# Optimization experiments

Measured on AMD Instinct MI355X. Metric: run time of the kernel, lower is better.

## Reference

```python
import jax, jax.numpy as jnp
import numpy as np

B, N, G, M = 16, 8192, 512, 32
ENC = 384   # encoder_dims
TRD = 384   # trans_dim (must equal ENC due to cls-pos concat)
EPS = 1e-5


def _fps(xyz, n_samples):
    # farthest point sampling: xyz [B,N,3] -> idx [B,n_samples] int32
    b, n, _ = xyz.shape
    def body(carry, _):
        dists, farthest = carry                       # [B,N], [B]
        centroid = jnp.take_along_axis(xyz, farthest[:, None, None], axis=1)  # [B,1,3]
        d = jnp.sum((xyz - centroid) ** 2, -1)        # [B,N]
        dists = jnp.minimum(dists, d)
        nxt = jnp.argmax(dists, -1).astype(jnp.int32)
        return (dists, nxt), farthest
    init = (jnp.full((b, n), 1e10, xyz.dtype), jnp.zeros((b,), jnp.int32))
    _, idxs = jax.lax.scan(body, init, None, length=n_samples)
    return idxs.T                                     # [B,n_samples]


def _group(pts):
    # FPS centers + kNN neighborhoods, neighborhood recentered on its center
    fps_idx = _fps(pts, G)                                    # [B,G]
    center = jax.vmap(lambda p, i: p[i])(pts, fps_idx)        # [B,G,3]
    d2 = jnp.sum((center[:, :, None, :] - pts[:, None, :, :]) ** 2, -1)  # [B,G,N]
    _, knn_idx = jax.lax.top_k(-d2, M)                        # [B,G,M]
    nbhd = jax.vmap(lambda p, i: p[i])(pts, knn_idx)          # [B,G,M,3]
    nbhd = nbhd - center[:, :, None, :]
    return nbhd, center


def _bn(x, g, b, m, v):
    return (x - m) * jax.lax.rsqrt(v + EPS) * g + b


def _forward(pts, W1, b1, g1, be1, m1, v1, W2, b2,
             W3, b3, g2, be2, m2, v2, W4, b4,
             Wp1, bp1, Wp2, bp2, cls_pos):
    nbhd, center = _group(pts)                                # [B,G,M,3], [B,G,3]
    # Encoder (Point-MAE, BN in eval mode)
    f = jnp.einsum('bgmc,cd->bgmd', nbhd, W1) + b1            # [B,G,M,128]
    f = jax.nn.relu(_bn(f, g1, be1, m1, v1))
    f = jnp.einsum('bgmc,cd->bgmd', f, W2) + b2               # [B,G,M,256]
    fg = jnp.max(f, axis=2, keepdims=True)                    # [B,G,1,256]
    f = jnp.concatenate([jnp.broadcast_to(fg, f.shape), f], -1)  # [B,G,M,512]
    f = jnp.einsum('bgmc,cd->bgmd', f, W3) + b3
    f = jax.nn.relu(_bn(f, g2, be2, m2, v2))
    f = jnp.einsum('bgmc,cd->bgmd', f, W4) + b4               # [B,G,M,ENC]
    x = jnp.max(f, axis=2)                                    # [B,G,ENC]
    # pos embed MLP on centers
    pos = jax.nn.gelu(center @ Wp1 + bp1) @ Wp2 + bp2         # [B,G,TRD]
    cls = jnp.broadcast_to(cls_pos, (pts.shape[0], 1, ENC))
    pos = jnp.concatenate([cls, pos], axis=1)                 # [B,G+1,TRD]
    return x, pos


def setup_inputs() -> dict:
    key = jax.random.key(0)
    ks = jax.random.split(key, 20)
    nrm = lambda k, s, sc: jax.random.normal(k, s, jnp.float32) * sc
    uni = lambda k, s: jax.random.uniform(k, s, jnp.float32, 0.5, 1.5)
    return {
        'pts': jax.random.normal(ks[0], (B, N, 3), jnp.float32),
        'W1': nrm(ks[1], (3, 128), 0.1), 'b1': jnp.zeros((128,), jnp.float32),
        'g1': uni(ks[2], (128,)), 'be1': nrm(ks[3], (128,), 0.1),
        'm1': nrm(ks[4], (128,), 0.1), 'v1': uni(ks[5], (128,)),
        'W2': nrm(ks[6], (128, 256), 0.05), 'b2': jnp.zeros((256,), jnp.float32),
        'W3': nrm(ks[7], (512, 512), 0.04), 'b3': jnp.zeros((512,), jnp.float32),
        'g2': uni(ks[8], (512,)), 'be2': nrm(ks[9], (512,), 0.1),
        'm2': nrm(ks[10], (512,), 0.1), 'v2': uni(ks[11], (512,)),
        'W4': nrm(ks[12], (512, ENC), 0.04), 'b4': jnp.zeros((ENC,), jnp.float32),
        'Wp1': nrm(ks[13], (3, 128), 0.1), 'bp1': jnp.zeros((128,), jnp.float32),
        'Wp2': nrm(ks[14], (128, TRD), 0.08), 'bp2': jnp.zeros((TRD,), jnp.float32),
        'cls_pos': nrm(ks[15], (1, 1, ENC), 0.02),
    }


def reference(pts, W1, b1, g1, be1, m1, v1, W2, b2, W3, b3, g2, be2, m2, v2,
              W4, b4, Wp1, bp1, Wp2, bp2, cls_pos):
    return _forward(pts, W1, b1, g1, be1, m1, v1, W2, b2, W3, b3, g2, be2,
                    m2, v2, W4, b4, Wp1, bp1, Wp2, bp2, cls_pos)
```

## Files before the change

### kernel.cpp

```cpp
#include <hip/hip_runtime.h>

typedef _Float16 f16;
typedef _Float16 f16x8 __attribute__((ext_vector_type(8)));
typedef float    f32x4 __attribute__((ext_vector_type(4)));

#define NB   16
#define NP   8192
#define NG   512
#define NM   32
#define ENC  384
#define NROWS (NB * NG * NM)

__device__ __forceinline__ void gl_lds16(const void* g, void* l) {
  __builtin_amdgcn_global_load_lds((const __attribute__((address_space(1))) unsigned int*)g,
                                   (__attribute__((address_space(3))) unsigned int*)l, 16, 0, 0);
}

__device__ __forceinline__ unsigned long long kmax(unsigned long long a, unsigned long long b) {
  return a > b ? a : b;
}
__device__ __forceinline__ unsigned long long kmin(unsigned long long a, unsigned long long b) {
  return a < b ? a : b;
}

template <int CTRL>
__device__ __forceinline__ unsigned long long dpp_kmax(unsigned long long k) {
  int lo = (int)(unsigned)(k & 0xFFFFFFFFull);
  int hi = (int)(unsigned)(k >> 32);
  int olo = __builtin_amdgcn_update_dpp(lo, lo, CTRL, 0xF, 0xF, false);
  int ohi = __builtin_amdgcn_update_dpp(hi, hi, CTRL, 0xF, 0xF, false);
  unsigned long long o = ((unsigned long long)(unsigned)ohi << 32) | (unsigned)olo;
  return kmax(k, o);
}
template <int CTRL>
__device__ __forceinline__ unsigned long long dpp_kmin(unsigned long long k) {
  int lo = (int)(unsigned)(k & 0xFFFFFFFFull);
  int hi = (int)(unsigned)(k >> 32);
  int olo = __builtin_amdgcn_update_dpp(lo, lo, CTRL, 0xF, 0xF, false);
  int ohi = __builtin_amdgcn_update_dpp(hi, hi, CTRL, 0xF, 0xF, false);
  unsigned long long o = ((unsigned long long)(unsigned)ohi << 32) | (unsigned)olo;
  return kmin(k, o);
}
__device__ __forceinline__ unsigned long long swz16_kmax(unsigned long long k) {
  int lo = (int)(unsigned)(k & 0xFFFFFFFFull);
  int hi = (int)(unsigned)(k >> 32);
  int olo = __builtin_amdgcn_ds_swizzle(lo, 0x401F);
  int ohi = __builtin_amdgcn_ds_swizzle(hi, 0x401F);
  unsigned long long o = ((unsigned long long)(unsigned)ohi << 32) | (unsigned)olo;
  return kmax(k, o);
}
__device__ __forceinline__ unsigned long long swz16_kmin(unsigned long long k) {
  int lo = (int)(unsigned)(k & 0xFFFFFFFFull);
  int hi = (int)(unsigned)(k >> 32);
  int olo = __builtin_amdgcn_ds_swizzle(lo, 0x401F);
  int ohi = __builtin_amdgcn_ds_swizzle(hi, 0x401F);
  unsigned long long o = ((unsigned long long)(unsigned)ohi << 32) | (unsigned)olo;
  return kmin(k, o);
}

#define DPP_QUAD_XOR1 0xB1
#define DPP_QUAD_XOR2 0x4E
#define DPP_HALF_MIRR 0x141
#define DPP_ROW_MIRR  0x140

__global__ __launch_bounds__(512) void fps_kernel(const float* __restrict__ pts,
                                                  float* __restrict__ centers) {
#pragma clang fp contract(off)
  const int b = blockIdx.x;
  const float* pb = pts + (size_t)b * NP * 3;
  const int t = threadIdx.x;
  const int lane = t & 63, wid = t >> 6;
  __shared__ float spx[NP], spy[NP], spz[NP];
  __shared__ unsigned long long swk[2][16];
  float px[16], py[16], pz[16], dd[16];
#pragma unroll
  for (int i = 0; i < 16; ++i) {
    int idx = t + i * 512;
    float x = pb[idx * 3 + 0], y = pb[idx * 3 + 1], z = pb[idx * 3 + 2];
    px[i] = x; py[i] = y; pz[i] = z; dd[i] = 1e10f;
    spx[idx] = x; spy[idx] = y; spz[idx] = z;
  }
  __syncthreads();
  float cx = spx[0], cy = spy[0], cz = spz[0];
  for (int g = 0; g < NG; ++g) {
    if (t == 0) {
      float* c = centers + ((size_t)b * NG + g) * 3;
      c[0] = cx; c[1] = cy; c[2] = cz;
    }
    float best = -1.0f; int bslot = 0;
#pragma unroll
    for (int i = 0; i < 16; ++i) {
      float dx = __fsub_rn(px[i], cx);
      float dy = __fsub_rn(py[i], cy);
      float dz = __fsub_rn(pz[i], cz);
      float d  = __fadd_rn(__fadd_rn(__fmul_rn(dx, dx), __fmul_rn(dy, dy)), __fmul_rn(dz, dz));
      dd[i] = fminf(dd[i], d);
      if (dd[i] > best) { best = dd[i]; bslot = i; }
    }
    int bidx = t + bslot * 512;
    unsigned long long key =
        ((unsigned long long)__float_as_uint(best) << 13) | (unsigned)(8191 - bidx);
    key = dpp_kmax<DPP_QUAD_XOR1>(key);
    key = dpp_kmax<DPP_QUAD_XOR2>(key);
    key = dpp_kmax<DPP_HALF_MIRR>(key);
    key = dpp_kmax<DPP_ROW_MIRR>(key);
    key = swz16_kmax(key);
    const int p = g & 1;
    if ((lane & 31) == 0) swk[p][wid * 2 + (lane >> 5)] = key;
    __syncthreads();
    unsigned long long k2 = swk[p][lane & 15];
    k2 = dpp_kmax<DPP_QUAD_XOR1>(k2);
    k2 = dpp_kmax<DPP_QUAD_XOR2>(k2);
    k2 = dpp_kmax<DPP_HALF_MIRR>(k2);
    k2 = dpp_kmax<DPP_ROW_MIRR>(k2);
    int widx = 8191 - (int)(k2 & 0x1FFFull);
    cx = spx[widx]; cy = spy[widx]; cz = spz[widx];
  }
}

__global__ __launch_bounds__(256) void knn_kernel(const float* __restrict__ pts,
                                                  const float* __restrict__ centers,
                                                  int* __restrict__ knn_idx) {
#pragma clang fp contract(off)
  const int gg = blockIdx.x;
  const int b = gg >> 9;
  const float* pb = pts + (size_t)b * NP * 3;
  const float* c = centers + (size_t)gg * 3;
  const float cx = c[0], cy = c[1], cz = c[2];
  __shared__ unsigned long long swk[2][8];
  const int t = threadIdx.x, lane = t & 63, wid = t >> 6;
  float d[32];
  float lmin = 3e38f; int lidx = 0;
#pragma unroll
  for (int i = 0; i < 32; ++i) {
    int idx = i * 256 + t;
    float dx = __fsub_rn(cx, pb[idx * 3 + 0]);
    float dy = __fsub_rn(cy, pb[idx * 3 + 1]);
    float dz = __fsub_rn(cz, pb[idx * 3 + 2]);
    d[i] = __fadd_rn(__fadd_rn(__fmul_rn(dx, dx), __fmul_rn(dy, dy)), __fmul_rn(dz, dz));
    if (d[i] < lmin) { lmin = d[i]; lidx = idx; }
  }
  int* outp = knn_idx + (size_t)gg * NM;
  for (int r = 0; r < NM; ++r) {
    unsigned long long key =
        ((unsigned long long)__float_as_uint(lmin) << 13) | (unsigned)lidx;
    key = dpp_kmin<DPP_QUAD_XOR1>(key);
    key = dpp_kmin<DPP_QUAD_XOR2>(key);
    key = dpp_kmin<DPP_HALF_MIRR>(key);
    key = dpp_kmin<DPP_ROW_MIRR>(key);
    key = swz16_kmin(key);
    const int p = r & 1;
    if ((lane & 31) == 0) swk[p][wid * 2 + (lane >> 5)] = key;
    __syncthreads();
    unsigned long long k2 = swk[p][lane & 7];
    k2 = dpp_kmin<DPP_QUAD_XOR1>(k2);
    k2 = dpp_kmin<DPP_QUAD_XOR2>(k2);
    k2 = dpp_kmin<DPP_HALF_MIRR>(k2);
    int i0 = (int)(k2 & 0x1FFFull);
    if (t == 0) outp[r] = i0;
    if ((i0 & 255) == t) {
      int slot = i0 >> 8;
      lmin = 3e38f; lidx = 0;
#pragma unroll
      for (int i = 0; i < 32; ++i) {
        float di = (i == slot) ? 3e38f : d[i];
        d[i] = di;
        if (di < lmin) { lmin = di; lidx = i * 256 + t; }
      }
    }
  }
}

__global__ void quant_kernel(const float* __restrict__ W2, const float* __restrict__ W3,
                             const float* __restrict__ W4, const float* __restrict__ Wp2,
                             const float* __restrict__ b1, const float* __restrict__ g1,
                             const float* __restrict__ be1, const float* __restrict__ m1,
                             const float* __restrict__ v1, const float* __restrict__ g2,
                             const float* __restrict__ be2, const float* __restrict__ m2,
                             const float* __restrict__ v2,
                             f16* __restrict__ W2T, f16* __restrict__ W3aT,
                             f16* __restrict__ W3bT, f16* __restrict__ W4T,
                             f16* __restrict__ Wp2T,
                             float* __restrict__ s1, float* __restrict__ sh1,
                             float* __restrict__ s2, float* __restrict__ sh2) {
  int i = blockIdx.x * 256 + threadIdx.x;
  if (i < 32768) { int n = i >> 7, k = i & 127; W2T[i] = (f16)W2[(size_t)k * 256 + n]; return; }
  i -= 32768;
  if (i < 131072) { int n = i >> 8, k = i & 255; W3aT[i] = (f16)W3[(size_t)k * 512 + n]; return; }
  i -= 131072;
  if (i < 131072) { int n = i >> 8, k = i & 255; W3bT[i] = (f16)W3[(size_t)(256 + k) * 512 + n]; return; }
  i -= 131072;
  if (i < 196608) { int n = i >> 9, k = i & 511; W4T[i] = (f16)W4[(size_t)k * 384 + n]; return; }
  i -= 196608;
  if (i < 49152) { int n = i >> 7, k = i & 127; Wp2T[i] = (f16)Wp2[(size_t)k * 384 + n]; return; }
  i -= 49152;
  if (i < 128) {
    float s = g1[i] * rsqrtf(v1[i] + 1e-5f);
    s1[i] = s; sh1[i] = (b1[i] - m1[i]) * s + be1[i];
    return;
  }
  i -= 128;
  if (i < 512) {
    float s = g2[i] * rsqrtf(v2[i] + 1e-5f);
    s2[i] = s; sh2[i] = be2[i] - m2[i] * s;
    return;
  }
}

template <int WRITE_F2>
__global__ __launch_bounds__(256) void l2f_kernel(const float* __restrict__ pts,
                                                  const float* __restrict__ centers,
                                                  const int* __restrict__ knn_idx,
                                                  const float* __restrict__ W1,
                                                  const float* __restrict__ s1,
                                                  const float* __restrict__ sh1,
                                                  const f16* __restrict__ W2T,
                                                  const float* __restrict__ b2,
                                                  f16* __restrict__ fg,
                                                  f16* __restrict__ f2, int grow0) {
  __shared__ __align__(16) f16 sF1[128 * 128];
  __shared__ float snb[128][3];
  const int t = threadIdx.x, lane = t & 63, wid = t >> 6;
  const int wr = wid >> 1, wc = wid & 1;
  const int l15 = lane & 15, lhi = lane >> 4;
  const int grow = grow0 + blockIdx.x * 128;
  const int y = blockIdx.y;

  if (t < 128) {
    int row = grow + t;
    int gg = row >> 5;
    int b = gg >> 9;
    int idx = knn_idx[(size_t)gg * NM + (row & 31)];
    const float* p = pts + ((size_t)b * NP + idx) * 3;
    const float* c = centers + (size_t)gg * 3;
    snb[t][0] = p[0] - c[0];
    snb[t][1] = p[1] - c[1];
    snb[t][2] = p[2] - c[2];
  }
  __syncthreads();
  {
    int row = t >> 1, c0 = (t & 1) * 64;
    float nx = snb[row][0], ny = snb[row][1], nz = snb[row][2];
    int sw = (row & 7) << 4;
#pragma unroll
    for (int cc = 0; cc < 64; cc += 8) {
      f16x8 v;
#pragma unroll
      for (int j = 0; j < 8; ++j) {
        int c = c0 + cc + j;
        float a = nx * W1[c] + ny * W1[128 + c] + nz * W1[256 + c];
        a = a * s1[c] + sh1[c];
        v[j] = (f16)fmaxf(a, 0.0f);
      }
      *(f16x8*)((char*)sF1 + row * 256 + (((c0 + cc) * 2) ^ sw)) = v;
    }
  }
  __syncthreads();

  f32x4 acc[4][4];
#pragma unroll
  for (int m = 0; m < 4; ++m)
#pragma unroll
    for (int n = 0; n < 4; ++n) acc[m][n] = (f32x4){0.f, 0.f, 0.f, 0.f};

  const f16* Wb = W2T + (size_t)(y * 128) * 128;
#pragma unroll
  for (int ks = 0; ks < 4; ++ks) {
    f16x8 af[4], bf[4];
#pragma unroll
    for (int m = 0; m < 4; ++m) {
      int row = wr * 64 + m * 16 + l15;
      af[m] = *(const f16x8*)((const char*)sF1 + row * 256 + ((ks * 64 + lhi * 16) ^ ((row & 7) << 4)));
    }
#pragma unroll
    for (int n = 0; n < 4; ++n) {
      int nr = wc * 64 + n * 16 + l15;
      bf[n] = *(const f16x8*)(Wb + (size_t)nr * 128 + ks * 32 + lhi * 8);
    }
#pragma unroll
    for (int m = 0; m < 4; ++m)
#pragma unroll
      for (int n = 0; n < 4; ++n)
        acc[m][n] = __builtin_amdgcn_mfma_f32_16x16x32_f16(af[m], bf[n], acc[m][n], 0, 0, 0);
  }

  float bias[4];
#pragma unroll
  for (int n = 0; n < 4; ++n) bias[n] = b2[y * 128 + wc * 64 + n * 16 + l15];
#pragma unroll
  for (int p = 0; p < 2; ++p) {
#pragma unroll
    for (int n = 0; n < 4; ++n) {
      float v = acc[2 * p][n][0];
#pragma unroll
      for (int i = 1; i < 4; ++i) v = fmaxf(v, acc[2 * p][n][i]);
#pragma unroll
      for (int i = 0; i < 4; ++i) v = fmaxf(v, acc[2 * p + 1][n][i]);
      v = fmaxf(v, __shfl_xor(v, 16));
      v = fmaxf(v, __shfl_xor(v, 32));
      if (lhi == 0)
        fg[(size_t)((grow >> 5) + wr * 2 + p) * 256 + y * 128 + wc * 64 + n * 16 + l15] =
            (f16)(v + bias[n]);
    }
  }

  if (WRITE_F2) {
    __syncthreads();
    f16* sF2 = sF1;
#pragma unroll
    for (int n = 0; n < 4; ++n) {
      int col = wc * 64 + n * 16 + l15;
#pragma unroll
      for (int m = 0; m < 4; ++m)
#pragma unroll
        for (int i = 0; i < 4; ++i) {
          int row = wr * 64 + m * 16 + lhi * 4 + i;
          sF2[row * 128 + col] = (f16)(acc[m][n][i] + bias[n]);
        }
    }
    __syncthreads();
#pragma unroll
    for (int ch = 0; ch < 8; ++ch) {
      int off = ch * 4096 + t * 16;
      int row = off >> 8, cb = off & 255;
      *(uint4*)((char*)f2 + (size_t)(blockIdx.x * 128 + row) * 512 + y * 256 + cb) =
          *(const uint4*)((const char*)sF2 + off);
    }
  }
}

template <int K, int EPI>
__global__ __launch_bounds__(256) void gemm128_kernel(const f16* __restrict__ A,
                                                      const f16* __restrict__ BT,
                                                      float* __restrict__ outF32,
                                                      f16* __restrict__ outF16,
                                                      const float* __restrict__ e0,
                                                      const float* __restrict__ e1,
                                                      const float* __restrict__ e2,
                                                      int NTOT, int gg0) {
  __shared__ __align__(16) f16 sA[128 * 64];
  __shared__ __align__(16) f16 sB[128 * 64];
  const int t = threadIdx.x, lane = t & 63, wid = t >> 6;
  const int wrow = wid >> 1, wcol = wid & 1;
  const int l15 = lane & 15, lhi = lane >> 4;
  f32x4 acc[4][4];
#pragma unroll
  for (int m = 0; m < 4; ++m)
#pragma unroll
    for (int n = 0; n < 4; ++n) acc[m][n] = (f32x4){0.f, 0.f, 0.f, 0.f};

  const size_t arow0 = (size_t)blockIdx.x * 128;
  const int ncol0 = blockIdx.y * 128;
  const char* Ab = (const char*)A;
  const char* Bb = (const char*)BT;
  const int so = wid * 1024 + lane * 16;
  const int cb = so & 127;
  const int r0 = so >> 7;

  for (int kt = 0; kt < K; kt += 64) {
#pragma unroll
    for (int rnd = 0; rnd < 4; ++rnd) {
      int r = rnd * 32 + r0;
      int sw = (r & 7) << 4;
      gl_lds16(Ab + (arow0 + r) * (size_t)(K * 2) + kt * 2 + (cb ^ sw),
               (char*)sA + rnd * 4096 + wid * 1024);
      gl_lds16(Bb + (size_t)(ncol0 + r) * (K * 2) + kt * 2 + (cb ^ sw),
               (char*)sB + rnd * 4096 + wid * 1024);
    }
    __syncthreads();
#pragma unroll
    for (int ks = 0; ks < 2; ++ks) {
      f16x8 af[4], bf[4];
#pragma unroll
      for (int m = 0; m < 4; ++m) {
        int row = wrow * 64 + m * 16 + l15;
        int addr = row * 128 + ((ks * 64 + lhi * 16) ^ ((row & 7) << 4));
        af[m] = *(const f16x8*)((const char*)sA + addr);
      }
#pragma unroll
      for (int n = 0; n < 4; ++n) {
        int nrow = wcol * 64 + n * 16 + l15;
        int addr = nrow * 128 + ((ks * 64 + lhi * 16) ^ ((nrow & 7) << 4));
        bf[n] = *(const f16x8*)((const char*)sB + addr);
      }
#pragma unroll
      for (int m = 0; m < 4; ++m)
#pragma unroll
        for (int n = 0; n < 4; ++n)
          acc[m][n] = __builtin_amdgcn_mfma_f32_16x16x32_f16(af[m], bf[n], acc[m][n], 0, 0, 0);
    }
    __syncthreads();
  }

  if (EPI == 1) {
#pragma unroll
    for (int n = 0; n < 4; ++n) {
      int col = ncol0 + wcol * 64 + n * 16 + l15;
      float s = e1[col], sh = e2[col];
#pragma unroll
      for (int m = 0; m < 4; ++m) {
        int grp = gg0 + blockIdx.x * 4 + wrow * 2 + (m >> 1);
        float gv = e0[(size_t)grp * 512 + col];
#pragma unroll
        for (int i = 0; i < 4; ++i) {
          size_t row = arow0 + wrow * 64 + m * 16 + lhi * 4 + i;
          float v = (acc[m][n][i] + gv) * s + sh;
          outF16[row * NTOT + col] = (f16)fmaxf(v, 0.0f);
        }
      }
    }
  } else if (EPI == 2) {
#pragma unroll
    for (int pr = 0; pr < 2; ++pr) {
      size_t gg_glob = (size_t)gg0 + blockIdx.x * 4 + wrow * 2 + pr;
#pragma unroll
      for (int n = 0; n < 4; ++n) {
        float v = acc[2 * pr][n][0];
#pragma unroll
        for (int i = 1; i < 4; ++i) v = fmaxf(v, acc[2 * pr][n][i]);
#pragma unroll
        for (int i = 0; i < 4; ++i) v = fmaxf(v, acc[2 * pr + 1][n][i]);
        v = fmaxf(v, __shfl_xor(v, 16));
        v = fmaxf(v, __shfl_xor(v, 32));
        if (lhi == 0) {
          int col = ncol0 + wcol * 64 + n * 16 + l15;
          outF32[gg_glob * ENC + col] = v + e0[col];
        }
      }
    }
  } else if (EPI == 3) {
#pragma unroll
    for (int n = 0; n < 4; ++n) {
      int col = ncol0 + wcol * 64 + n * 16 + l15;
      float bias = e0[col];
#pragma unroll
      for (int m = 0; m < 4; ++m)
#pragma unroll
        for (int i = 0; i < 4; ++i) {
          size_t row = arow0 + wrow * 64 + m * 16 + lhi * 4 + i;
          outF32[row * NTOT + col] = acc[m][n][i] + bias;
        }
    }
  } else {
#pragma unroll
    for (int n = 0; n < 4; ++n) {
      int col = ncol0 + wcol * 64 + n * 16 + l15;
      float bias = e0[col];
#pragma unroll
      for (int m = 0; m < 4; ++m)
#pragma unroll
        for (int i = 0; i < 4; ++i) {
          size_t row = arow0 + wrow * 64 + m * 16 + lhi * 4 + i;
          int b = (int)(row >> 9), g = (int)(row & 511);
          outF32[((size_t)b * 513 + 1 + g) * 384 + col] = acc[m][n][i] + bias;
        }
    }
  }
}

__global__ __launch_bounds__(256) void posh_kernel(const float* __restrict__ centers,
                                                   const float* __restrict__ Wp1,
                                                   const float* __restrict__ bp1,
                                                   f16* __restrict__ h) {
  int o = blockIdx.x * 256 + threadIdx.x;
  int row = o >> 7, c = o & 127;
  const float* ct = centers + (size_t)row * 3;
  float x = ct[0] * Wp1[c] + ct[1] * Wp1[128 + c] + ct[2] * Wp1[256 + c] + bp1[c];
  float u = 0.7978845608028654f * (x + 0.044715f * x * x * x);
  h[o] = (f16)(0.5f * x * (1.0f + tanhf(u)));
}

__global__ void cls_kernel(const float* __restrict__ cls_pos, float* __restrict__ out_pos) {
  out_pos[(size_t)blockIdx.x * (NG + 1) * ENC + threadIdx.x] = cls_pos[threadIdx.x];
}

extern "C" void kernel_launch(void* const* d_in, const int* in_sizes, int n_in,
                              void* d_out, int out_size, void* d_ws, size_t ws_size,
                              hipStream_t stream) {
  const float* pts = (const float*)d_in[0];
  const float* W1  = (const float*)d_in[1];
  const float* b1  = (const float*)d_in[2];
  const float* g1  = (const float*)d_in[3];
  const float* be1 = (const float*)d_in[4];
  const float* m1  = (const float*)d_in[5];
  const float* v1  = (const float*)d_in[6];
  const float* W2  = (const float*)d_in[7];
  const float* b2  = (const float*)d_in[8];
  const float* W3  = (const float*)d_in[9];
  const float* b3  = (const float*)d_in[10];
  const float* g2  = (const float*)d_in[11];
  const float* be2 = (const float*)d_in[12];
  const float* m2  = (const float*)d_in[13];
  const float* v2  = (const float*)d_in[14];
  const float* W4  = (const float*)d_in[15];
  const float* b4  = (const float*)d_in[16];
  const float* Wp1 = (const float*)d_in[17];
  const float* bp1 = (const float*)d_in[18];
  const float* Wp2 = (const float*)d_in[19];
  const float* bp2 = (const float*)d_in[20];
  const float* cls = (const float*)d_in[21];

  float* out_x   = (float*)d_out;
  float* out_pos = out_x + (size_t)NB * NG * ENC;

  char* w = (char*)d_ws;
  auto alloc = [&](size_t bytes) {
    char* p = w;
    w += (bytes + 255) & ~(size_t)255;
    return p;
  };
  float* centers = (float*)alloc((size_t)NB * NG * 3 * 4);
  int*   knn     = (int*)alloc((size_t)NB * NG * NM * 4);
  f16*   W2T     = (f16*)alloc(32768 * 2);
  f16*   W3aT    = (f16*)alloc(131072 * 2);
  f16*   W3bT    = (f16*)alloc(131072 * 2);
  f16*   W4T     = (f16*)alloc(196608 * 2);
  f16*   Wp2T    = (f16*)alloc(49152 * 2);
  float* s1      = (float*)alloc(128 * 4);
  float* sh1     = (float*)alloc(128 * 4);
  float* s2      = (float*)alloc(512 * 4);
  float* sh2     = (float*)alloc(512 * 4);
  f16*   fg      = (f16*)alloc((size_t)8192 * 256 * 2);
  float* g3      = (float*)alloc((size_t)8192 * 512 * 4);
  f16*   h       = (f16*)alloc((size_t)8192 * 128 * 2);
  size_t fixed = (size_t)(w - (char*)d_ws);
  const size_t f2_full = (size_t)NROWS * 256 * 2;
  const size_t f3_full = (size_t)NROWS * 512 * 2;

  quant_kernel<<<dim3(2115), dim3(256), 0, stream>>>(W2, W3, W4, Wp2, b1, g1, be1, m1, v1,
                                                     g2, be2, m2, v2, W2T, W3aT, W3bT, W4T,
                                                     Wp2T, s1, sh1, s2, sh2);
  fps_kernel<<<dim3(NB), dim3(512), 0, stream>>>(pts, centers);
  knn_kernel<<<dim3(NB * NG), dim3(256), 0, stream>>>(pts, centers, knn);

  if (ws_size >= fixed + f2_full + f3_full / 4 + 4096) {
    f16* f2  = (f16*)alloc(f2_full);
    f16* f3c = (f16*)alloc(f3_full / 4);
    l2f_kernel<1><<<dim3(2048, 2), dim3(256), 0, stream>>>(pts, centers, knn, W1, s1, sh1,
                                                           W2T, b2, fg, f2, 0);
    gemm128_kernel<256, 3><<<dim3(64, 4), dim3(256), 0, stream>>>(
        fg, W3aT, g3, nullptr, b3, nullptr, nullptr, 512, 0);
    for (int c = 0; c < 4; ++c) {
      gemm128_kernel<256, 1><<<dim3(512, 4), dim3(256), 0, stream>>>(
          f2 + (size_t)c * 65536 * 256, W3bT, nullptr, f3c, g3, s2, sh2, 512, c * 2048);
      gemm128_kernel<512, 2><<<dim3(512, 3), dim3(256), 0, stream>>>(
          f3c, W4T, out_x, nullptr, b4, nullptr, nullptr, 384, c * 2048);
    }
  } else {
    f16* f2c = (f16*)alloc((size_t)32768 * 256 * 2);
    f16* f3c = (f16*)alloc((size_t)32768 * 512 * 2);
    l2f_kernel<0><<<dim3(2048, 2), dim3(256), 0, stream>>>(pts, centers, knn, W1, s1, sh1,
                                                           W2T, b2, fg, nullptr, 0);
    gemm128_kernel<256, 3><<<dim3(64, 4), dim3(256), 0, stream>>>(
        fg, W3aT, g3, nullptr, b3, nullptr, nullptr, 512, 0);
    for (int c = 0; c < 8; ++c) {
      l2f_kernel<1><<<dim3(256, 2), dim3(256), 0, stream>>>(pts, centers, knn, W1, s1, sh1,
                                                            W2T, b2, fg, f2c, c * 32768);
      gemm128_kernel<256, 1><<<dim3(256, 4), dim3(256), 0, stream>>>(
          f2c, W3bT, nullptr, f3c, g3, s2, sh2, 512, c * 1024);
      gemm128_kernel<512, 2><<<dim3(256, 3), dim3(256), 0, stream>>>(
          f3c, W4T, out_x, nullptr, b4, nullptr, nullptr, 384, c * 1024);
    }
  }

  posh_kernel<<<dim3(4096), dim3(256), 0, stream>>>(centers, Wp1, bp1, h);
  gemm128_kernel<128, 4><<<dim3(64, 3), dim3(256), 0, stream>>>(
      h, Wp2T, out_pos, nullptr, bp2, nullptr, nullptr, 384, 0);
  cls_kernel<<<dim3(NB), dim3(ENC), 0, stream>>>(cls, out_pos);
}
```

Before: 1.185 ms.

## Double-buffer GEMM LDS tiles and process encoder rows in larger chunks

The 128x128 MFMA GEMM now keeps two LDS buffers for A and B. It issues the global-to-LDS loads for the next K tile before computing on the current one, and uses explicit vmcnt waits and barriers instead of full __syncthreads. The host also gains a new path that, when the workspace is large enough, splits the f3 intermediate into two chunks instead of four, halving the number of GEMM launch pairs. The aim is to overlap memory latency with MFMA work and cut launch and tail overhead, at the cost of doubling LDS use (64 KB per block), which may lower occupancy.

```diff
diff --git a/kernel.cpp b/kernel.cpp
--- a/kernel.cpp
+++ b/kernel.cpp
@@ -338,8 +338,8 @@
                                                       const float* __restrict__ e1,
                                                       const float* __restrict__ e2,
                                                       int NTOT, int gg0) {
-  __shared__ __align__(16) f16 sA[128 * 64];
-  __shared__ __align__(16) f16 sB[128 * 64];
+  __shared__ __align__(16) f16 sA[2][128 * 64];
+  __shared__ __align__(16) f16 sB[2][128 * 64];
   const int t = threadIdx.x, lane = t & 63, wid = t >> 6;
   const int wrow = wid >> 1, wcol = wid & 1;
   const int l15 = lane & 15, lhi = lane >> 4;
@@ -356,18 +356,31 @@
   const int so = wid * 1024 + lane * 16;
   const int cb = so & 127;
   const int r0 = so >> 7;
-
-  for (int kt = 0; kt < K; kt += 64) {
+  const int KSTEPS = K / 64;
+
+  auto STAGE = [&](int bsel, int kt) {
 #pragma unroll
     for (int rnd = 0; rnd < 4; ++rnd) {
       int r = rnd * 32 + r0;
       int sw = (r & 7) << 4;
-      gl_lds16(Ab + (arow0 + r) * (size_t)(K * 2) + kt * 2 + (cb ^ sw),
-               (char*)sA + rnd * 4096 + wid * 1024);
-      gl_lds16(Bb + (size_t)(ncol0 + r) * (K * 2) + kt * 2 + (cb ^ sw),
-               (char*)sB + rnd * 4096 + wid * 1024);
-    }
-    __syncthreads();
+      gl_lds16(Ab + (arow0 + r) * (size_t)(K * 2) + kt * 128 + (cb ^ sw),
+               (char*)sA[bsel] + rnd * 4096 + wid * 1024);
+      gl_lds16(Bb + (size_t)(ncol0 + r) * (K * 2) + kt * 128 + (cb ^ sw),
+               (char*)sB[bsel] + rnd * 4096 + wid * 1024);
+    }
+  };
+
+  STAGE(0, 0);
+  int cur = 0;
+#pragma unroll
+  for (int kt = 0; kt < KSTEPS; ++kt) {
+    if (kt + 1 < KSTEPS) {
+      STAGE(cur ^ 1, kt + 1);
+      asm volatile("s_waitcnt vmcnt(8)" ::: "memory");
+    } else {
+      asm volatile("s_waitcnt vmcnt(0)" ::: "memory");
+    }
+    __builtin_amdgcn_s_barrier();
 #pragma unroll
     for (int ks = 0; ks < 2; ++ks) {
       f16x8 af[4], bf[4];
@@ -375,13 +388,13 @@
       for (int m = 0; m < 4; ++m) {
         int row = wrow * 64 + m * 16 + l15;
         int addr = row * 128 + ((ks * 64 + lhi * 16) ^ ((row & 7) << 4));
-        af[m] = *(const f16x8*)((const char*)sA + addr);
+        af[m] = *(const f16x8*)((const char*)sA[cur] + addr);
       }
 #pragma unroll
       for (int n = 0; n < 4; ++n) {
         int nrow = wcol * 64 + n * 16 + l15;
         int addr = nrow * 128 + ((ks * 64 + lhi * 16) ^ ((nrow & 7) << 4));
-        bf[n] = *(const f16x8*)((const char*)sB + addr);
+        bf[n] = *(const f16x8*)((const char*)sB[cur] + addr);
       }
 #pragma unroll
       for (int m = 0; m < 4; ++m)
@@ -389,7 +402,9 @@
         for (int n = 0; n < 4; ++n)
           acc[m][n] = __builtin_amdgcn_mfma_f32_16x16x32_f16(af[m], bf[n], acc[m][n], 0, 0, 0);
     }
-    __syncthreads();
+    asm volatile("" ::: "memory");
+    __builtin_amdgcn_s_barrier();
+    cur ^= 1;
   }
 
   if (EPI == 1) {
@@ -533,7 +548,20 @@
   fps_kernel<<<dim3(NB), dim3(512), 0, stream>>>(pts, centers);
   knn_kernel<<<dim3(NB * NG), dim3(256), 0, stream>>>(pts, centers, knn);
 
-  if (ws_size >= fixed + f2_full + f3_full / 4 + 4096) {
+  if (ws_size >= fixed + f2_full + f3_full / 2 + 4096) {
+    f16* f2  = (f16*)alloc(f2_full);
+    f16* f3c = (f16*)alloc(f3_full / 2);
+    l2f_kernel<1><<<dim3(2048, 2), dim3(256), 0, stream>>>(pts, centers, knn, W1, s1, sh1,
+                                                           W2T, b2, fg, f2, 0);
+    gemm128_kernel<256, 3><<<dim3(64, 4), dim3(256), 0, stream>>>(
+        fg, W3aT, g3, nullptr, b3, nullptr, nullptr, 512, 0);
+    for (int c = 0; c < 2; ++c) {
+      gemm128_kernel<256, 1><<<dim3(1024, 4), dim3(256), 0, stream>>>(
+          f2 + (size_t)c * 131072 * 256, W3bT, nullptr, f3c, g3, s2, sh2, 512, c * 4096);
+      gemm128_kernel<512, 2><<<dim3(1024, 3), dim3(256), 0, stream>>>(
+          f3c, W4T, out_x, nullptr, b4, nullptr, nullptr, 384, c * 4096);
+    }
+  } else if (ws_size >= fixed + f2_full + f3_full / 4 + 4096) {
     f16* f2  = (f16*)alloc(f2_full);
     f16* f3c = (f16*)alloc(f3_full / 4);
     l2f_kernel<1><<<dim3(2048, 2), dim3(256), 0, stream>>>(pts, centers, knn, W1, s1, sh1,
```

Result: faster. 1.125 ms (median of 2 runs) (-5.1%).
